# Optimization experiments

Measured on AMD Instinct MI355X. Metric: run time of the kernel, lower is better.

## Reference

```python
import jax, jax.numpy as jnp
import numpy as np

B, L, D, H = 2, 4096, 768, 12
HS = D // H  # head_size = 64
SCALE = HS ** -0.5


def setup_inputs() -> dict:
    key = jax.random.key(0)
    k1, k2, k3 = jax.random.split(key, 3)
    x = jax.random.normal(k1, (B, L, D), dtype=jnp.float32)
    # torch nn.Linear weights are [out_features, in_features]; y = x @ W.T
    Wq = jax.random.normal(k2, (D, D), dtype=jnp.float32) * (D ** -0.5)
    Wo = jax.random.normal(k3, (D, D), dtype=jnp.float32) * (D ** -0.5)
    return {"x": x, "Wq": Wq, "Wo": Wo}


def reference(x, Wq, Wo):
    b, l, d = x.shape
    # NOTE: source module uses self.query for Q, K, AND V (bug preserved).
    q = jnp.einsum('bld,ed->ble', x, Wq)              # [B,L,D]
    q = q.reshape(b, l, H, HS).transpose(0, 2, 1, 3)   # [B,H,L,HS]
    k = v = q                                          # K = V = Q (faithful)
    scores = jnp.einsum('bhqd,bhkd->bhqk', q, k) * SCALE  # [B,H,L,L]
    attn = jax.nn.softmax(scores, axis=-1)
    out = jnp.einsum('bhqk,bhkd->bhqd', attn, v)       # [B,H,L,HS]
    out = out.transpose(0, 2, 1, 3).reshape(b, l, d)   # [B,L,D]
    out = jnp.einsum('bld,ed->ble', out, Wo)           # output projection
    return out
```

## Files before the change

### kernel.cpp

```cpp
#include <hip/hip_runtime.h>
#include <hip/hip_bf16.h>

#define LQ 4096
#define DQ 768
#define NH 12
#define NB 2

typedef __attribute__((ext_vector_type(8))) short short8;
typedef __attribute__((ext_vector_type(2))) unsigned uint2v;
typedef __attribute__((ext_vector_type(4))) float f32x4;

__device__ __forceinline__ short f2bf(float f) {
    union { float f; unsigned u; } v; v.f = f;
    unsigned r = v.u + 0x7FFFu + ((v.u >> 16) & 1u);
    return (short)(r >> 16);
}

__device__ __forceinline__ unsigned pk2(float a, float b) {
    float2 t; t.x = a; t.y = b;
    __hip_bfloat162 h = __float22bfloat162_rn(t);
    unsigned u; __builtin_memcpy(&u, &h, 4);
    return u;
}

__device__ __forceinline__ f32x4 mfma16(short8 a, short8 b, f32x4 c) {
    return __builtin_amdgcn_mfma_f32_16x16x32_bf16(a, b, c, 0, 0, 0);
}

__device__ __forceinline__ void gld16(const short* g, short* l) {
    __builtin_amdgcn_global_load_lds(
        (const __attribute__((address_space(1))) unsigned int*)(g),
        (__attribute__((address_space(3))) unsigned int*)(l), 16, 0, 0);
}

#define SQRT_C 0.424660891f

__global__ __launch_bounds__(256) void cvtw(const float* __restrict__ a,
                                            short* __restrict__ o) {
    int i = blockIdx.x * 256 + threadIdx.x;
    float4 v = ((const float4*)a)[i];
    *(uint2v*)&o[i * 4] = (uint2v){pk2(v.x, v.y), pk2(v.z, v.w)};
}


template <int MODE>
__global__ __launch_bounds__(512, 2) void gemm_nt(const short* __restrict__ A,
                                                  const short* __restrict__ Wb,
                                                  void* __restrict__ Cp,
                                                  short* __restrict__ Vf) {
    __shared__ __attribute__((aligned(16))) short smem[40960];
    const int t = threadIdx.x;
    const int lane = t & 63, w = t >> 6;
    const int lr = lane & 15, qd = lane >> 4;
    const int wm = (w >> 2) * 64, wn = (w & 3) * 48;
    const int lin = blockIdx.x;
    const int xcd = lin & 7, jj = lin >> 3;
    const int nt = jj & 3, mt = (jj >> 2) * 8 + xcd;
    const int m0 = mt * 128, n0 = nt * 192;

    int aoffs[2], boffs[3];
#pragma unroll
    for (int u = 0; u < 2; ++u) {
        int c = (u * 8 + w) * 64 + lane;
        int row = c >> 3, k = (c & 7) ^ (row & 7);
        aoffs[u] = (m0 + row) * DQ + k * 8;
    }
#pragma unroll
    for (int u = 0; u < 3; ++u) {
        int c = (u * 8 + w) * 64 + lane;
        int row = c >> 3, k = (c & 7) ^ (row & 7);
        boffs[u] = (n0 + row) * DQ + k * 8;
    }

    f32x4 acc[4][3];
#pragma unroll
    for (int i = 0; i < 4; ++i)
#pragma unroll
        for (int j = 0; j < 3; ++j) acc[i][j] = (f32x4){0.f, 0.f, 0.f, 0.f};

#pragma unroll
    for (int u = 0; u < 2; ++u) gld16(&A[aoffs[u]], &smem[(u * 8 + w) * 512]);
#pragma unroll
    for (int u = 0; u < 3; ++u) gld16(&Wb[boffs[u]], &smem[16384 + (u * 8 + w) * 512]);
    __syncthreads();

    int cur = 0;
    for (int kt = 0; kt < 12; ++kt) {
        if (kt < 11) {
            const int k0 = (kt + 1) * 64;
#pragma unroll
            for (int u = 0; u < 2; ++u)
                gld16(&A[aoffs[u] + k0], &smem[(cur ^ 1) * 8192 + (u * 8 + w) * 512]);
#pragma unroll
            for (int u = 0; u < 3; ++u)
                gld16(&Wb[boffs[u] + k0], &smem[16384 + (cur ^ 1) * 12288 + (u * 8 + w) * 512]);
        }
        const short* Asb = &smem[cur * 8192];
        const short* Bsb = &smem[16384 + cur * 12288];
#pragma unroll
        for (int s = 0; s < 2; ++s) {
            const int cq = ((4 * s + qd) ^ (lr & 7)) * 8;
            short8 af[4], bf[3];
#pragma unroll
            for (int i = 0; i < 4; ++i)
                af[i] = *(const short8*)&Asb[(wm + 16 * i + lr) * 64 + cq];
#pragma unroll
            for (int j = 0; j < 3; ++j)
                bf[j] = *(const short8*)&Bsb[(wn + 16 * j + lr) * 64 + cq];
#pragma unroll
            for (int i = 0; i < 4; ++i)
#pragma unroll
                for (int j = 0; j < 3; ++j)
                    acc[i][j] = mfma16(af[i], bf[j], acc[i][j]);
        }
        __syncthreads();
        cur ^= 1;
    }

    if (MODE == 0) {
#pragma unroll
        for (int i = 0; i < 4; ++i)
#pragma unroll
            for (int j = 0; j < 3; ++j) {
                const int row0 = m0 + wm + 16 * i + qd * 4;
                const int col = n0 + wn + 16 * j + lr;
#pragma unroll
                for (int r = 0; r < 4; ++r)
                    ((float*)Cp)[(size_t)(row0 + r) * DQ + col] = acc[i][j][r];
            }
    } else {
        short* Qf = (short*)Cp;
        short* F = smem;
        const int bh0 = (m0 >> 12) * NH + nt * 3;
        const int kl0 = m0 & 4095;
#pragma unroll
        for (int i = 0; i < 4; ++i)
#pragma unroll
            for (int j = 0; j < 3; ++j) {
                const int kl = wm + 16 * i + qd * 4;
                const int hsg = wn + 16 * j + lr;
                const int hh = hsg >> 6, hs = hsg & 63;
                const int fi = hh * 8192 + ((kl >> 6) & 1) * 4096
                             + ((((hs >> 4) << 1) + ((kl >> 5) & 1)) << 9)
                             + (((hs & 15) + (((kl >> 3) & 3) << 4)) << 3) + (kl & 7);
                *(uint2v*)&F[fi] = (uint2v){pk2(acc[i][j][0], acc[i][j][1]),
                                            pk2(acc[i][j][2], acc[i][j][3])};
            }
        __syncthreads();
#pragma unroll
        for (int p = 0; p < 6; ++p) {
            int u = t + 512 * p;
            int hh = u >> 10, rem = u & 1023;
            size_t g = (size_t)(bh0 + hh) * (LQ * 64) + (size_t)((kl0 >> 6) << 12);
            *(short8*)&Vf[g + (size_t)rem * 8] = *(short8*)&F[u * 8];
        }
        __syncthreads();
#pragma unroll
        for (int i = 0; i < 4; ++i)
#pragma unroll
            for (int j = 0; j < 3; ++j) {
                const int hsg = wn + 16 * j + lr;
                const int hh = hsg >> 6, hs = hsg & 63;
#pragma unroll
                for (int r = 0; r < 4; ++r) {
                    const int key = wm + 16 * i + qd * 4 + r;
                    const int fi = hh * 8192 + ((key >> 6) & 1) * 4096
                                 + (((((key >> 4) & 3) << 1) + (hs >> 5)) << 9)
                                 + (((qd * 4 + r) + (((hs >> 3) & 3) << 4)) << 3) + (hs & 7);
                    F[fi] = f2bf(acc[i][j][r] * SQRT_C);
                }
            }
        __syncthreads();
#pragma unroll
        for (int p = 0; p < 6; ++p) {
            int u = t + 512 * p;
            int hh = u >> 10, rem = u & 1023;
            size_t g = (size_t)(bh0 + hh) * (LQ * 64) + (size_t)((kl0 >> 6) << 12);
            *(short8*)&Qf[g + (size_t)rem * 8] = *(short8*)&F[u * 8];
        }
    }
}

__global__ __launch_bounds__(256, 3) void attn(const short* __restrict__ Qf,
                                               const short* __restrict__ Vf,
                                               short* __restrict__ O) {
    const int linear = blockIdx.x;
    const int xcd = linear & 7, slot = linear >> 3;
    const int bh = 3 * xcd + (slot >> 5);
    const int qtile = slot & 31;
    const int t = threadIdx.x;
    const int lane = t & 63, w = t >> 6;
    const int qw = w & 1, half = w >> 1;
    const int lr = lane & 15, qd = lane >> 4;

    __shared__ alignas(16) char smem[43008];
    short* aqs = (short*)smem;
    short* Ps = (short*)(smem + 16384) + w * 2560;

    const short* Qbh = Qf + (size_t)bh * (LQ * 64);
    const short* Vbh = Vf + (size_t)bh * (LQ * 64);
    const int q0 = qtile * 128 + qw * 64;
    const int kb0 = half * 64;

    const short one_bf = (short)0x3F80;
    short8 ones;
#pragma unroll
    for (int j = 0; j < 8; ++j) ones[j] = one_bf;

#pragma unroll
    for (int p = 0; p < 4; ++p) {
        int off = (t + 256 * p) * 8;
        *(short8*)&aqs[off] = *(const short8*)&Qbh[(size_t)qtile * 8192 + off];
    }
    __syncthreads();

    f32x4 oacc[4][4], lacc[4];
#pragma unroll
    for (int i = 0; i < 4; ++i) {
        lacc[i] = (f32x4){0.f, 0.f, 0.f, 0.f};
#pragma unroll
        for (int t2 = 0; t2 < 4; ++t2) oacc[i][t2] = (f32x4){0.f, 0.f, 0.f, 0.f};
    }

    const int aqbase = qw * 4096 + lane * 8;

    for (int kb = kb0; kb < kb0 + 64; ++kb) {
        short8 kf[2][2];
#pragma unroll
        for (int t4 = 0; t4 < 2; ++t4)
#pragma unroll
            for (int s = 0; s < 2; ++s)
                kf[t4][s] = *(const short8*)&Qbh[kb * 2048 + (t4 * 2 + s) * 512 + lane * 8];

#pragma unroll
        for (int i = 0; i < 4; ++i) {
            short8 aq0 = *(const short8*)&aqs[aqbase + i * 1024];
            short8 aq1 = *(const short8*)&aqs[aqbase + i * 1024 + 512];
            f32x4 s0 = (f32x4){0.f, 0.f, 0.f, 0.f};
            f32x4 s1 = (f32x4){0.f, 0.f, 0.f, 0.f};
            s0 = mfma16(kf[0][0], aq0, s0);
            s0 = mfma16(kf[0][1], aq1, s0);
            s1 = mfma16(kf[1][0], aq0, s1);
            s1 = mfma16(kf[1][1], aq1, s1);
            *(uint2v*)&Ps[i * 640 + lr * 40 + 4 * qd] =
                (uint2v){pk2(__builtin_amdgcn_exp2f(s0[0]), __builtin_amdgcn_exp2f(s0[1])),
                         pk2(__builtin_amdgcn_exp2f(s0[2]), __builtin_amdgcn_exp2f(s0[3]))};
            *(uint2v*)&Ps[i * 640 + lr * 40 + 16 + 4 * qd] =
                (uint2v){pk2(__builtin_amdgcn_exp2f(s1[0]), __builtin_amdgcn_exp2f(s1[1])),
                         pk2(__builtin_amdgcn_exp2f(s1[2]), __builtin_amdgcn_exp2f(s1[3]))};
        }

        short8 vb[4];
#pragma unroll
        for (int t2 = 0; t2 < 4; ++t2)
            vb[t2] = *(const short8*)&Vbh[(kb >> 1) * 4096 + (kb & 1) * 512 + t2 * 1024 + lane * 8];

#pragma unroll
        for (int i = 0; i < 4; ++i) {
            short8 pa = *(short8*)&Ps[i * 640 + lr * 40 + qd * 8];
#pragma unroll
            for (int t2 = 0; t2 < 4; ++t2)
                oacc[i][t2] = mfma16(pa, vb[t2], oacc[i][t2]);
            lacc[i] = mfma16(pa, ones, lacc[i]);
        }
    }

    __syncthreads();
    f32x4* ex = (f32x4*)smem + (qw * 64 + lane) * 21;
    if (half) {
#pragma unroll
        for (int i = 0; i < 4; ++i) {
#pragma unroll
            for (int t2 = 0; t2 < 4; ++t2) ex[i * 4 + t2] = oacc[i][t2];
            ex[16 + i] = lacc[i];
        }
    }
    __syncthreads();
    if (half) return;

#pragma unroll
    for (int i = 0; i < 4; ++i) {
#pragma unroll
        for (int t2 = 0; t2 < 4; ++t2) oacc[i][t2] += ex[i * 4 + t2];
        lacc[i] += ex[16 + i];
    }

    const int b = bh / NH, h = bh % NH;
#pragma unroll
    for (int i = 0; i < 4; ++i) {
        float inv[4];
#pragma unroll
        for (int r = 0; r < 4; ++r) inv[r] = 1.0f / lacc[i][r];
#pragma unroll
        for (int t2 = 0; t2 < 4; ++t2)
#pragma unroll
            for (int r = 0; r < 4; ++r) {
                int lq = q0 + 16 * i + qd * 4 + r;
                int e = h * 64 + 16 * t2 + lr;
                O[((size_t)(b * LQ + lq)) * DQ + e] = f2bf(oacc[i][t2][r] * inv[r]);
            }
    }
}

extern "C" void kernel_launch(void* const* d_in, const int* in_sizes, int n_in,
                              void* d_out, int out_size, void* d_ws, size_t ws_size,
                              hipStream_t stream) {
    (void)in_sizes; (void)n_in; (void)out_size; (void)ws_size;
    const float* x  = (const float*)d_in[0];
    const float* Wq = (const float*)d_in[1];
    const float* Wo = (const float*)d_in[2];
    float* out = (float*)d_out;

    const size_t NQ = (size_t)NB * NH * LQ * 64;
    const size_t NW = (size_t)DQ * DQ;
    short* Qf  = (short*)d_ws;
    short* Vfb = Qf + NQ;
    short* Ows = Vfb + NQ;
    short* Wqb = Ows + (size_t)NB * LQ * DQ;
    short* Wob = Wqb + NW;

    cvtw<<<(NB * LQ * DQ) / 1024, 256, 0, stream>>>(x, Ows);
    cvtw<<<NW / 1024, 256, 0, stream>>>(Wq, Wqb);
    cvtw<<<NW / 1024, 256, 0, stream>>>(Wo, Wob);
    gemm_nt<1><<<256, 512, 0, stream>>>(Ows, Wqb, Qf, Vfb);
    attn<<<768, 256, 0, stream>>>(Qf, Vfb, Ows);
    gemm_nt<0><<<256, 512, 0, stream>>>(Ows, Wob, out, nullptr);
}
```

Baseline: 233.3 us.

## Fuse fp32-to-bf16 conversion of x and weights into GEMM tile loads

Removes the three standalone conversion kernels and instead loads fp32 x and weights directly in the GEMMs, converting to bf16 in registers and writing to LDS. The next k-tile is prefetched into registers before the MFMA loop and stored to LDS afterward, replacing the async global_load_lds path for those operands. This removes three launches and the extra round trip through workspace, but doubles the global bytes per tile and adds register pressure and VALU conversion work inside the GEMM main loop.

```diff
diff --git a/kernel.cpp b/kernel.cpp
--- a/kernel.cpp
+++ b/kernel.cpp
@@ -8,6 +8,7 @@
 
 typedef __attribute__((ext_vector_type(8))) short short8;
 typedef __attribute__((ext_vector_type(2))) unsigned uint2v;
+typedef __attribute__((ext_vector_type(4))) unsigned uint4v;
 typedef __attribute__((ext_vector_type(4))) float f32x4;
 
 __device__ __forceinline__ short f2bf(float f) {
@@ -35,17 +36,11 @@
 
 #define SQRT_C 0.424660891f
 
-__global__ __launch_bounds__(256) void cvtw(const float* __restrict__ a,
-                                            short* __restrict__ o) {
-    int i = blockIdx.x * 256 + threadIdx.x;
-    float4 v = ((const float4*)a)[i];
-    *(uint2v*)&o[i * 4] = (uint2v){pk2(v.x, v.y), pk2(v.z, v.w)};
-}
-
 
 template <int MODE>
-__global__ __launch_bounds__(512, 2) void gemm_nt(const short* __restrict__ A,
-                                                  const short* __restrict__ Wb,
+__global__ __launch_bounds__(512, 2) void gemm_nt(const short* __restrict__ Abf,
+                                                  const float* __restrict__ Axf,
+                                                  const float* __restrict__ Wf,
                                                   void* __restrict__ Cp,
                                                   short* __restrict__ Vf) {
     __shared__ __attribute__((aligned(16))) short smem[40960];
@@ -58,18 +53,29 @@
     const int nt = jj & 3, mt = (jj >> 2) * 8 + xcd;
     const int m0 = mt * 128, n0 = nt * 192;
 
-    int aoffs[2], boffs[3];
-#pragma unroll
-    for (int u = 0; u < 2; ++u) {
-        int c = (u * 8 + w) * 64 + lane;
-        int row = c >> 3, k = (c & 7) ^ (row & 7);
-        aoffs[u] = (m0 + row) * DQ + k * 8;
-    }
+    int aoffs[2];
+    if (MODE == 0) {
+#pragma unroll
+        for (int u = 0; u < 2; ++u) {
+            int c = (u * 8 + w) * 64 + lane;
+            int row = c >> 3, k = (c & 7) ^ (row & 7);
+            aoffs[u] = (m0 + row) * DQ + k * 8;
+        }
+    } else {
+#pragma unroll
+        for (int u = 0; u < 2; ++u) {
+            int c = t + 512 * u;
+            int row = c >> 3, k = (c & 7) ^ (row & 7);
+            aoffs[u] = (m0 + row) * DQ + k * 8;
+        }
+    }
+    int boffs[3], bdst[3];
 #pragma unroll
     for (int u = 0; u < 3; ++u) {
-        int c = (u * 8 + w) * 64 + lane;
+        int c = t + 512 * u;
         int row = c >> 3, k = (c & 7) ^ (row & 7);
         boffs[u] = (n0 + row) * DQ + k * 8;
+        bdst[u] = c * 8;
     }
 
     f32x4 acc[4][3];
@@ -78,22 +84,48 @@
 #pragma unroll
         for (int j = 0; j < 3; ++j) acc[i][j] = (f32x4){0.f, 0.f, 0.f, 0.f};
 
-#pragma unroll
-    for (int u = 0; u < 2; ++u) gld16(&A[aoffs[u]], &smem[(u * 8 + w) * 512]);
-#pragma unroll
-    for (int u = 0; u < 3; ++u) gld16(&Wb[boffs[u]], &smem[16384 + (u * 8 + w) * 512]);
+    if (MODE == 0) {
+#pragma unroll
+        for (int u = 0; u < 2; ++u) gld16(&Abf[aoffs[u]], &smem[(u * 8 + w) * 512]);
+    } else {
+#pragma unroll
+        for (int u = 0; u < 2; ++u) {
+            float4 lo = *(const float4*)&Axf[aoffs[u]];
+            float4 hi = *(const float4*)&Axf[aoffs[u] + 4];
+            *(uint4v*)&smem[(t + 512 * u) * 8] =
+                (uint4v){pk2(lo.x, lo.y), pk2(lo.z, lo.w), pk2(hi.x, hi.y), pk2(hi.z, hi.w)};
+        }
+    }
+#pragma unroll
+    for (int u = 0; u < 3; ++u) {
+        float4 lo = *(const float4*)&Wf[boffs[u]];
+        float4 hi = *(const float4*)&Wf[boffs[u] + 4];
+        *(uint4v*)&smem[16384 + bdst[u]] =
+            (uint4v){pk2(lo.x, lo.y), pk2(lo.z, lo.w), pk2(hi.x, hi.y), pk2(hi.z, hi.w)};
+    }
     __syncthreads();
 
     int cur = 0;
     for (int kt = 0; kt < 12; ++kt) {
+        float4 fa[2][2], fb[3][2];
         if (kt < 11) {
             const int k0 = (kt + 1) * 64;
-#pragma unroll
-            for (int u = 0; u < 2; ++u)
-                gld16(&A[aoffs[u] + k0], &smem[(cur ^ 1) * 8192 + (u * 8 + w) * 512]);
-#pragma unroll
-            for (int u = 0; u < 3; ++u)
-                gld16(&Wb[boffs[u] + k0], &smem[16384 + (cur ^ 1) * 12288 + (u * 8 + w) * 512]);
+            if (MODE == 0) {
+#pragma unroll
+                for (int u = 0; u < 2; ++u)
+                    gld16(&Abf[aoffs[u] + k0], &smem[(cur ^ 1) * 8192 + (u * 8 + w) * 512]);
+            } else {
+#pragma unroll
+                for (int u = 0; u < 2; ++u) {
+                    fa[u][0] = *(const float4*)&Axf[aoffs[u] + k0];
+                    fa[u][1] = *(const float4*)&Axf[aoffs[u] + k0 + 4];
+                }
+            }
+#pragma unroll
+            for (int u = 0; u < 3; ++u) {
+                fb[u][0] = *(const float4*)&Wf[boffs[u] + k0];
+                fb[u][1] = *(const float4*)&Wf[boffs[u] + k0 + 4];
+            }
         }
         const short* Asb = &smem[cur * 8192];
         const short* Bsb = &smem[16384 + cur * 12288];
@@ -112,6 +144,20 @@
 #pragma unroll
                 for (int j = 0; j < 3; ++j)
                     acc[i][j] = mfma16(af[i], bf[j], acc[i][j]);
+        }
+        if (kt < 11) {
+            if (MODE == 1) {
+#pragma unroll
+                for (int u = 0; u < 2; ++u)
+                    *(uint4v*)&smem[(cur ^ 1) * 8192 + (t + 512 * u) * 8] =
+                        (uint4v){pk2(fa[u][0].x, fa[u][0].y), pk2(fa[u][0].z, fa[u][0].w),
+                                 pk2(fa[u][1].x, fa[u][1].y), pk2(fa[u][1].z, fa[u][1].w)};
+            }
+#pragma unroll
+            for (int u = 0; u < 3; ++u)
+                *(uint4v*)&smem[16384 + (cur ^ 1) * 12288 + bdst[u]] =
+                    (uint4v){pk2(fb[u][0].x, fb[u][0].y), pk2(fb[u][0].z, fb[u][0].w),
+                             pk2(fb[u][1].x, fb[u][1].y), pk2(fb[u][1].z, fb[u][1].w)};
         }
         __syncthreads();
         cur ^= 1;
@@ -312,17 +358,11 @@
     float* out = (float*)d_out;
 
     const size_t NQ = (size_t)NB * NH * LQ * 64;
-    const size_t NW = (size_t)DQ * DQ;
     short* Qf  = (short*)d_ws;
     short* Vfb = Qf + NQ;
     short* Ows = Vfb + NQ;
-    short* Wqb = Ows + (size_t)NB * LQ * DQ;
-    short* Wob = Wqb + NW;
-
-    cvtw<<<(NB * LQ * DQ) / 1024, 256, 0, stream>>>(x, Ows);
-    cvtw<<<NW / 1024, 256, 0, stream>>>(Wq, Wqb);
-    cvtw<<<NW / 1024, 256, 0, stream>>>(Wo, Wob);
-    gemm_nt<1><<<256, 512, 0, stream>>>(Ows, Wqb, Qf, Vfb);
+
+    gemm_nt<1><<<256, 512, 0, stream>>>(nullptr, x, Wq, Qf, Vfb);
     attn<<<768, 256, 0, stream>>>(Qf, Vfb, Ows);
-    gemm_nt<0><<<256, 512, 0, stream>>>(Ows, Wob, out, nullptr);
-}
+    gemm_nt<0><<<256, 512, 0, stream>>>(Ows, nullptr, Wo, out, nullptr);
+}
```

New measurement: 235.9 us. About the same (+1.1%).
